# Performance work log

Measured on AMD Instinct MI355X. Metric: run time of the kernel, lower is better.

Reference implementation:

```python
import jax, jax.numpy as jnp
import numpy as np

N_NODES = 100000
N_EDGES = 1600000
NODE_D = 64
EDGE_D = 48
U_D = 32
N_GRAPHS = 64
HIDDEN = 128
OUT_D = 64
IN_D = NODE_D + EDGE_D + U_D  # 144


def setup_inputs() -> dict:
    key = jax.random.key(0)
    ks = jax.random.split(key, 10)
    x = jax.random.normal(ks[0], (N_NODES, NODE_D), dtype=jnp.float32)
    edge_index = jax.random.randint(ks[1], (2, N_EDGES), 0, N_NODES, dtype=jnp.int64)
    edge_attr = jax.random.normal(ks[2], (N_EDGES, EDGE_D), dtype=jnp.float32)
    u = jax.random.normal(ks[3], (N_GRAPHS, U_D), dtype=jnp.float32)
    batch = jnp.sort(jax.random.randint(ks[4], (N_NODES,), 0, N_GRAPHS, dtype=jnp.int64))
    # FCNN params: Linear(144,128) -> relu -> Linear(128,128) -> relu -> Linear(128,64)
    W1 = jax.random.normal(ks[5], (IN_D, HIDDEN), dtype=jnp.float32) / np.sqrt(IN_D)
    b1 = jnp.zeros((HIDDEN,), dtype=jnp.float32)
    W2 = jax.random.normal(ks[6], (HIDDEN, HIDDEN), dtype=jnp.float32) / np.sqrt(HIDDEN)
    b2 = jnp.zeros((HIDDEN,), dtype=jnp.float32)
    W3 = jax.random.normal(ks[7], (HIDDEN, OUT_D), dtype=jnp.float32) / np.sqrt(HIDDEN)
    b3 = jnp.zeros((OUT_D,), dtype=jnp.float32)
    return {"x": x, "edge_index": edge_index, "edge_attr": edge_attr, "u": u,
            "batch": batch, "W1": W1, "b1": b1, "W2": W2, "b2": b2, "W3": W3, "b3": b3}


def reference(x, edge_index, edge_attr, u, batch, W1, b1, W2, b2, W3, b3):
    n = x.shape[0]
    seg = edge_index[0]  # source node per edge
    # scatter_mean(edge_attr, edge_index[0], dim=0) -> [N, edge_d]
    sums = jax.ops.segment_sum(edge_attr, seg, num_segments=n)
    cnt = jax.ops.segment_sum(jnp.ones((edge_attr.shape[0],), edge_attr.dtype), seg, num_segments=n)
    v_e = sums / jnp.maximum(cnt, 1.0)[:, None]  # mean, 0 for empty segments
    comb = jnp.concatenate([x, v_e, u[batch]], axis=1)  # [N, 144]
    h = jax.nn.relu(comb @ W1 + b1)
    h = jax.nn.relu(h @ W2 + b2)
    return h @ W3 + b3
```

## Files before the change

### kernel.cpp

```cpp
#include <hip/hip_runtime.h>
#include <hip/hip_bf16.h>

#define NN 100000
#define NE 1600000
#define NODE_D 64
#define EDGE_D 48
#define U_D 32
#define IN_D 144
#define HID 128
#define OUT_D 64
#define BM 64
#define S0 152
#define SCAN_BS 1024
#define SCAN_NB ((NN + SCAN_BS - 1) / SCAN_BS)
#define W1K 160
#define NW1 (HID * W1K)
#define NW2 (HID * HID)
#define NW3 (OUT_D * HID)
#define NWTOT (NW1 + NW2 + NW3)
#define IDS 1536

typedef __attribute__((ext_vector_type(8))) short bf16x8;
typedef __attribute__((ext_vector_type(4))) float f32x4;

__device__ __forceinline__ short f2bs(float f) {
  union { __hip_bfloat16 h; short s; } v;
  v.h = __float2bfloat16(f);
  return v.s;
}

__device__ __forceinline__ void st4(unsigned short* p, float4 v) {
  unsigned a = (unsigned)(unsigned short)f2bs(v.x) | ((unsigned)(unsigned short)f2bs(v.y) << 16);
  unsigned b = (unsigned)(unsigned short)f2bs(v.z) | ((unsigned)(unsigned short)f2bs(v.w) << 16);
  *reinterpret_cast<uint2*>(p) = make_uint2(a, b);
}

__global__ __launch_bounds__(256) void setup_kernel(
    int* __restrict__ hist,
    const float* __restrict__ W1, const float* __restrict__ W2,
    const float* __restrict__ W3, unsigned short* __restrict__ Wp) {
  const int b = blockIdx.x, tid = threadIdx.x;
  if (b < SCAN_NB) {
    int base = b * SCAN_BS + tid * 4;
    if (base + 3 < NN) {
      *reinterpret_cast<int4*>(&hist[base]) = make_int4(0, 0, 0, 0);
    } else {
      for (int k = 0; k < 4; ++k)
        if (base + k < NN) hist[base + k] = 0;
    }
    return;
  }
  int gid = (b - SCAN_NB) * 256 + tid;
  if (gid >= NWTOT) return;
  float v;
  if (gid < NW1) {
    int n = gid / W1K, k = gid - n * W1K;
    v = (k < IN_D) ? W1[(size_t)k * HID + n] : 0.f;
  } else if (gid < NW1 + NW2) {
    int i2 = gid - NW1;
    int n = i2 >> 7, k = i2 & 127;
    v = W2[(size_t)k * HID + n];
  } else {
    int i3 = gid - NW1 - NW2;
    int n = i3 >> 7, k = i3 & 127;
    v = W3[(size_t)k * OUT_D + n];
  }
  Wp[gid] = (unsigned short)f2bs(v);
}

__global__ __launch_bounds__(256) void hist_kernel(const int* __restrict__ src,
                                                   int* __restrict__ hist) {
  int i = blockIdx.x * 256 + threadIdx.x;
  if (i * 4 >= NE) return;
  int4 s = reinterpret_cast<const int4*>(src)[i];
  atomicAdd(&hist[s.x], 1);
  atomicAdd(&hist[s.y], 1);
  atomicAdd(&hist[s.z], 1);
  atomicAdd(&hist[s.w], 1);
}

__global__ __launch_bounds__(256) void bsum_kernel(const int* __restrict__ hist,
                                                   int* __restrict__ bsum) {
  const int b = blockIdx.x, tid = threadIdx.x;
  const int base = b * SCAN_BS + tid * 4;
  int4 v = make_int4(0, 0, 0, 0);
  if (base + 3 < NN) v = *reinterpret_cast<const int4*>(&hist[base]);
  else {
    int t[4] = {0, 0, 0, 0};
    for (int k = 0; k < 4; ++k) if (base + k < NN) t[k] = hist[base + k];
    v = make_int4(t[0], t[1], t[2], t[3]);
  }
  int s = v.x + v.y + v.z + v.w;
  for (int d = 32; d; d >>= 1) s += __shfl_down(s, d, 64);
  __shared__ int ws[4];
  if ((tid & 63) == 0) ws[tid >> 6] = s;
  __syncthreads();
  if (tid == 0) bsum[b] = ws[0] + ws[1] + ws[2] + ws[3];
}

__global__ __launch_bounds__(128) void bscan_kernel(const int* __restrict__ bsum,
                                                    int* __restrict__ bpre) {
  const int t = threadIdx.x;
  const int lane = t & 63, wave = t >> 6;
  int v = (t < SCAN_NB) ? bsum[t] : 0;
  int incl = v;
  for (int d = 1; d < 64; d <<= 1) {
    int q = __shfl_up(incl, d, 64);
    if (lane >= d) incl += q;
  }
  __shared__ int wtot[2];
  if (lane == 63) wtot[wave] = incl;
  __syncthreads();
  int add = (wave == 1) ? wtot[0] : 0;
  if (t < SCAN_NB) bpre[t] = incl - v + add;
}

__global__ __launch_bounds__(256) void offsets_kernel(const int* __restrict__ hist,
                                                      const int* __restrict__ bpre,
                                                      int* __restrict__ offsets,
                                                      int* __restrict__ cursor) {
  const int b = blockIdx.x, tid = threadIdx.x;
  const int base = b * SCAN_BS + tid * 4;
  const int lane = tid & 63, wave = tid >> 6;
  int4 v = make_int4(0, 0, 0, 0);
  if (base + 3 < NN) v = *reinterpret_cast<const int4*>(&hist[base]);
  else {
    int t[4] = {0, 0, 0, 0};
    for (int k = 0; k < 4; ++k) if (base + k < NN) t[k] = hist[base + k];
    v = make_int4(t[0], t[1], t[2], t[3]);
  }
  const int tsum = v.x + v.y + v.z + v.w;
  int incl = tsum;
  for (int d = 1; d < 64; d <<= 1) {
    int q = __shfl_up(incl, d, 64);
    if (lane >= d) incl += q;
  }
  __shared__ int ws[4];
  __shared__ int wpre[4];
  if (lane == 63) ws[wave] = incl;
  __syncthreads();
  if (tid == 0) {
    int r = 0;
    for (int w = 0; w < 4; ++w) { wpre[w] = r; r += ws[w]; }
  }
  __syncthreads();
  int run = bpre[b] + wpre[wave] + incl - tsum;
  int vals[4] = {v.x, v.y, v.z, v.w};
  for (int k = 0; k < 4; ++k) {
    int i = base + k;
    if (i < NN) { offsets[i] = run; cursor[i] = run; run += vals[k]; }
  }
}

__global__ __launch_bounds__(256) void permute_kernel(const int* __restrict__ src,
                                                      int* __restrict__ cursor,
                                                      int* __restrict__ perm) {
  int i = blockIdx.x * 256 + threadIdx.x;
  if (i * 4 >= NE) return;
  int4 s = reinterpret_cast<const int4*>(src)[i];
  const int e = i * 4;
  int p0 = atomicAdd(&cursor[s.x], 1);
  int p1 = atomicAdd(&cursor[s.y], 1);
  int p2 = atomicAdd(&cursor[s.z], 1);
  int p3 = atomicAdd(&cursor[s.w], 1);
  __builtin_nontemporal_store(e + 0, &perm[p0]);
  __builtin_nontemporal_store(e + 1, &perm[p1]);
  __builtin_nontemporal_store(e + 2, &perm[p2]);
  __builtin_nontemporal_store(e + 3, &perm[p3]);
}

__global__ __launch_bounds__(256) void fused_kernel(
    const float* __restrict__ x, const float* __restrict__ ea,
    const float* __restrict__ u, const int* __restrict__ batch,
    const int* __restrict__ perm, const int* __restrict__ hist,
    const int* __restrict__ offsets, const unsigned short* __restrict__ Wp,
    const float* __restrict__ b1, const float* __restrict__ b2,
    const float* __restrict__ b3, float* __restrict__ out) {
  __shared__ __align__(16) unsigned short act[BM][S0];
  __shared__ int ids[IDS];

  const int tid = threadIdx.x;
  const int lane = tid & 63;
  const int wid = tid >> 6;
  const int lr = lane & 15;
  const int lg = lane >> 4;
  const int node0 = blockIdx.x * BM;

  const unsigned short* Wp1 = Wp;
  const unsigned short* Wp2 = Wp + NW1;
  const unsigned short* Wp3 = Wp + NW1 + NW2;

  const bf16x8 az = {0, 0, 0, 0, 0, 0, 0, 0};

  const int start = offsets[node0];
  const int end = (node0 + BM < NN) ? offsets[node0 + BM] : NE;
  const int L = end - start;
  for (int i = tid; i < L && i < IDS; i += 256)
    ids[i] = perm[start + i];

  for (int i = tid; i < BM * (NODE_D / 4); i += 256) {
    int r = i >> 4, q = i & 15;
    int node = node0 + r;
    float4 v = make_float4(0.f, 0.f, 0.f, 0.f);
    if (node < NN) v = reinterpret_cast<const float4*>(x)[(size_t)node * 16 + q];
    st4(&act[r][q * 4], v);
  }
  for (int i = tid; i < BM * (U_D / 4); i += 256) {
    int r = i >> 3, q = i & 7;
    int node = node0 + r;
    float4 v = make_float4(0.f, 0.f, 0.f, 0.f);
    if (node < NN) {
      int b = batch[node];
      v = reinterpret_cast<const float4*>(u)[(size_t)b * 8 + q];
    }
    st4(&act[r][NODE_D + EDGE_D + q * 4], v);
  }
  __syncthreads();

  {
    const int g = tid >> 4;
    const int c = tid & 15;
    const bool on = (c < 12);
    const float* bc = ea + (size_t)c * 4;
    for (int i = 0; i < 4; ++i) {
      const int nl = g * 4 + i;
      const int node = node0 + nl;
      int deg = 0, sl = 0;
      if (node < NN) { deg = hist[node]; sl = offsets[node] - start; }
      float4 a0 = make_float4(0.f, 0.f, 0.f, 0.f);
      float4 a1 = make_float4(0.f, 0.f, 0.f, 0.f);
      int j = 0;
      for (; j + 7 < deg; j += 8) {
        int p = sl + j;
        int e0 = (p + 0 < IDS) ? ids[p + 0] : perm[start + p + 0];
        int e1 = (p + 1 < IDS) ? ids[p + 1] : perm[start + p + 1];
        int e2 = (p + 2 < IDS) ? ids[p + 2] : perm[start + p + 2];
        int e3 = (p + 3 < IDS) ? ids[p + 3] : perm[start + p + 3];
        int e4 = (p + 4 < IDS) ? ids[p + 4] : perm[start + p + 4];
        int e5 = (p + 5 < IDS) ? ids[p + 5] : perm[start + p + 5];
        int e6 = (p + 6 < IDS) ? ids[p + 6] : perm[start + p + 6];
        int e7 = (p + 7 < IDS) ? ids[p + 7] : perm[start + p + 7];
        if (on) {
          float4 v0 = *reinterpret_cast<const float4*>(bc + (size_t)e0 * EDGE_D);
          float4 v1 = *reinterpret_cast<const float4*>(bc + (size_t)e1 * EDGE_D);
          float4 v2 = *reinterpret_cast<const float4*>(bc + (size_t)e2 * EDGE_D);
          float4 v3 = *reinterpret_cast<const float4*>(bc + (size_t)e3 * EDGE_D);
          float4 v4 = *reinterpret_cast<const float4*>(bc + (size_t)e4 * EDGE_D);
          float4 v5 = *reinterpret_cast<const float4*>(bc + (size_t)e5 * EDGE_D);
          float4 v6 = *reinterpret_cast<const float4*>(bc + (size_t)e6 * EDGE_D);
          float4 v7 = *reinterpret_cast<const float4*>(bc + (size_t)e7 * EDGE_D);
          a0.x += (v0.x + v1.x) + (v2.x + v3.x);
          a0.y += (v0.y + v1.y) + (v2.y + v3.y);
          a0.z += (v0.z + v1.z) + (v2.z + v3.z);
          a0.w += (v0.w + v1.w) + (v2.w + v3.w);
          a1.x += (v4.x + v5.x) + (v6.x + v7.x);
          a1.y += (v4.y + v5.y) + (v6.y + v7.y);
          a1.z += (v4.z + v5.z) + (v6.z + v7.z);
          a1.w += (v4.w + v5.w) + (v6.w + v7.w);
        }
      }
      for (; j + 3 < deg; j += 4) {
        int p = sl + j;
        int e0 = (p + 0 < IDS) ? ids[p + 0] : perm[start + p + 0];
        int e1 = (p + 1 < IDS) ? ids[p + 1] : perm[start + p + 1];
        int e2 = (p + 2 < IDS) ? ids[p + 2] : perm[start + p + 2];
        int e3 = (p + 3 < IDS) ? ids[p + 3] : perm[start + p + 3];
        if (on) {
          float4 v0 = *reinterpret_cast<const float4*>(bc + (size_t)e0 * EDGE_D);
          float4 v1 = *reinterpret_cast<const float4*>(bc + (size_t)e1 * EDGE_D);
          float4 v2 = *reinterpret_cast<const float4*>(bc + (size_t)e2 * EDGE_D);
          float4 v3 = *reinterpret_cast<const float4*>(bc + (size_t)e3 * EDGE_D);
          a0.x += (v0.x + v1.x) + (v2.x + v3.x);
          a0.y += (v0.y + v1.y) + (v2.y + v3.y);
          a0.z += (v0.z + v1.z) + (v2.z + v3.z);
          a0.w += (v0.w + v1.w) + (v2.w + v3.w);
        }
      }
      for (; j < deg; ++j) {
        int p = sl + j;
        int e0 = (p < IDS) ? ids[p] : perm[start + p];
        if (on) {
          float4 v0 = *reinterpret_cast<const float4*>(bc + (size_t)e0 * EDGE_D);
          a0.x += v0.x; a0.y += v0.y; a0.z += v0.z; a0.w += v0.w;
        }
      }
      float inv = (deg > 0) ? 1.0f / (float)deg : 0.0f;
      if (on && node < NN)
        st4(&act[nl][NODE_D + c * 4],
            make_float4((a0.x + a1.x) * inv, (a0.y + a1.y) * inv,
                        (a0.z + a1.z) * inv, (a0.w + a1.w) * inv));
    }
  }
  __syncthreads();

  {
    const int n0 = wid * 32;
    bf16x8 wf[5][2];
#pragma unroll
    for (int t = 0; t < 5; ++t)
#pragma unroll
      for (int nf = 0; nf < 2; ++nf)
        wf[t][nf] = *reinterpret_cast<const bf16x8*>(
            &Wp1[(size_t)(n0 + nf * 16 + lr) * W1K + t * 32 + lg * 8]);
    float bias0 = b1[n0 + lr], bias1 = b1[n0 + 16 + lr];
    f32x4 acc[4][2];
#pragma unroll
    for (int mf = 0; mf < 4; ++mf) {
      acc[mf][0] = (f32x4){bias0, bias0, bias0, bias0};
      acc[mf][1] = (f32x4){bias1, bias1, bias1, bias1};
    }
#pragma unroll
    for (int t = 0; t < 5; ++t) {
#pragma unroll
      for (int mf = 0; mf < 4; ++mf) {
        bf16x8 a;
        if (t < 4) {
          a = *reinterpret_cast<const bf16x8*>(&act[mf * 16 + lr][t * 32 + lg * 8]);
        } else {
          a = az;
          if (lg < 2)
            a = *reinterpret_cast<const bf16x8*>(&act[mf * 16 + lr][128 + lg * 8]);
        }
        acc[mf][0] = __builtin_amdgcn_mfma_f32_16x16x32_bf16(a, wf[t][0], acc[mf][0], 0, 0, 0);
        acc[mf][1] = __builtin_amdgcn_mfma_f32_16x16x32_bf16(a, wf[t][1], acc[mf][1], 0, 0, 0);
      }
    }
    __syncthreads();
#pragma unroll
    for (int mf = 0; mf < 4; ++mf)
#pragma unroll
      for (int nf = 0; nf < 2; ++nf)
#pragma unroll
        for (int r = 0; r < 4; ++r)
          act[mf * 16 + lg * 4 + r][n0 + nf * 16 + lr] =
              (unsigned short)f2bs(fmaxf(acc[mf][nf][r], 0.f));
  }
  __syncthreads();

  {
    const int n0 = wid * 32;
    bf16x8 wf[4][2];
#pragma unroll
    for (int t = 0; t < 4; ++t)
#pragma unroll
      for (int nf = 0; nf < 2; ++nf)
        wf[t][nf] = *reinterpret_cast<const bf16x8*>(
            &Wp2[(size_t)(n0 + nf * 16 + lr) * HID + t * 32 + lg * 8]);
    float bias0 = b2[n0 + lr], bias1 = b2[n0 + 16 + lr];
    f32x4 acc[4][2];
#pragma unroll
    for (int mf = 0; mf < 4; ++mf) {
      acc[mf][0] = (f32x4){bias0, bias0, bias0, bias0};
      acc[mf][1] = (f32x4){bias1, bias1, bias1, bias1};
    }
#pragma unroll
    for (int t = 0; t < 4; ++t) {
#pragma unroll
      for (int mf = 0; mf < 4; ++mf) {
        bf16x8 a = *reinterpret_cast<const bf16x8*>(&act[mf * 16 + lr][t * 32 + lg * 8]);
        acc[mf][0] = __builtin_amdgcn_mfma_f32_16x16x32_bf16(a, wf[t][0], acc[mf][0], 0, 0, 0);
        acc[mf][1] = __builtin_amdgcn_mfma_f32_16x16x32_bf16(a, wf[t][1], acc[mf][1], 0, 0, 0);
      }
    }
    __syncthreads();
#pragma unroll
    for (int mf = 0; mf < 4; ++mf)
#pragma unroll
      for (int nf = 0; nf < 2; ++nf)
#pragma unroll
        for (int r = 0; r < 4; ++r)
          act[mf * 16 + lg * 4 + r][n0 + nf * 16 + lr] =
              (unsigned short)f2bs(fmaxf(acc[mf][nf][r], 0.f));
  }
  __syncthreads();

  {
    const int n0 = wid * 16;
    bf16x8 wf[4];
#pragma unroll
    for (int t = 0; t < 4; ++t)
      wf[t] = *reinterpret_cast<const bf16x8*>(
          &Wp3[(size_t)(n0 + lr) * HID + t * 32 + lg * 8]);
    float bias = b3[n0 + lr];
    f32x4 acc[4];
#pragma unroll
    for (int mf = 0; mf < 4; ++mf) acc[mf] = (f32x4){bias, bias, bias, bias};
#pragma unroll
    for (int t = 0; t < 4; ++t) {
#pragma unroll
      for (int mf = 0; mf < 4; ++mf) {
        bf16x8 a = *reinterpret_cast<const bf16x8*>(&act[mf * 16 + lr][t * 32 + lg * 8]);
        acc[mf] = __builtin_amdgcn_mfma_f32_16x16x32_bf16(a, wf[t], acc[mf], 0, 0, 0);
      }
    }
#pragma unroll
    for (int mf = 0; mf < 4; ++mf)
#pragma unroll
      for (int r = 0; r < 4; ++r) {
        int node = node0 + mf * 16 + lg * 4 + r;
        if (node < NN) out[(size_t)node * OUT_D + n0 + lr] = acc[mf][r];
      }
  }
}

extern "C" void kernel_launch(void* const* d_in, const int* in_sizes, int n_in,
                              void* d_out, int out_size, void* d_ws, size_t ws_size,
                              hipStream_t stream) {
  const float* x   = (const float*)d_in[0];
  const int* ei    = (const int*)d_in[1];
  const float* ea  = (const float*)d_in[2];
  const float* u   = (const float*)d_in[3];
  const int* batch = (const int*)d_in[4];
  const float* W1  = (const float*)d_in[5];
  const float* b1  = (const float*)d_in[6];
  const float* W2  = (const float*)d_in[7];
  const float* b2  = (const float*)d_in[8];
  const float* W3  = (const float*)d_in[9];
  const float* b3  = (const float*)d_in[10];
  float* out = (float*)d_out;

  int* hist    = (int*)d_ws;
  int* offsets = hist + NN;
  int* cursor  = offsets + NN;
  int* perm    = cursor + NN;
  int* bsum    = perm + NE;
  int* bpre    = bsum + SCAN_NB;
  unsigned short* Wp = (unsigned short*)(bpre + SCAN_NB + 60);

  const int wblocks = (NWTOT + 255) / 256;
  const int e4blocks = (NE / 4 + 255) / 256;
  setup_kernel<<<SCAN_NB + wblocks, 256, 0, stream>>>(hist, W1, W2, W3, Wp);
  hist_kernel<<<e4blocks, 256, 0, stream>>>(ei, hist);
  bsum_kernel<<<SCAN_NB, 256, 0, stream>>>(hist, bsum);
  bscan_kernel<<<1, 128, 0, stream>>>(bsum, bpre);
  offsets_kernel<<<SCAN_NB, 256, 0, stream>>>(hist, bpre, offsets, cursor);
  permute_kernel<<<e4blocks, 256, 0, stream>>>(ei, cursor, perm);
  fused_kernel<<<(NN + BM - 1) / BM, 256, 0, stream>>>(
      x, ea, u, batch, perm, hist, offsets, Wp, b1, b2, b3, out);
}
```

Measured before the change: 318.1 us.

## Scatter edge features into CSR-sorted bf16 buffer instead of index permutation

Instead of building a permutation of edge ids and gathering fp32 edge rows by index in the fused kernel, the permute stage now reads each edge's fp32 feature row and writes it as bf16 into its sorted CSR slot. The fused kernel then reads each node's edges contiguously in bf16, dropping the shared-memory id staging, the perm lookups and one barrier. The edge array is read once in its original order, then written and re-read at half width. The cost is an extra 154MB-class scatter write pass plus a larger workspace, and edge features are rounded to bf16 before averaging, which adds rounding error.

```diff
diff --git a/kernel.cpp b/kernel.cpp
--- a/kernel.cpp
+++ b/kernel.cpp
@@ -18,15 +18,21 @@
 #define NW2 (HID * HID)
 #define NW3 (OUT_D * HID)
 #define NWTOT (NW1 + NW2 + NW3)
-#define IDS 1536
 
 typedef __attribute__((ext_vector_type(8))) short bf16x8;
 typedef __attribute__((ext_vector_type(4))) float f32x4;
+typedef __attribute__((ext_vector_type(4))) unsigned int u32x4;
 
 __device__ __forceinline__ short f2bs(float f) {
   union { __hip_bfloat16 h; short s; } v;
   v.h = __float2bfloat16(f);
   return v.s;
+}
+__device__ __forceinline__ float blo(unsigned int pk) {
+  union { unsigned int u; float f; } v; v.u = pk << 16; return v.f;
+}
+__device__ __forceinline__ float bhi(unsigned int pk) {
+  union { unsigned int u; float f; } v; v.u = pk & 0xffff0000u; return v.f;
 }
 
 __device__ __forceinline__ void st4(unsigned short* p, float4 v) {
@@ -152,32 +158,41 @@
   }
 }
 
-__global__ __launch_bounds__(256) void permute_kernel(const int* __restrict__ src,
-                                                      int* __restrict__ cursor,
-                                                      int* __restrict__ perm) {
-  int i = blockIdx.x * 256 + threadIdx.x;
-  if (i * 4 >= NE) return;
-  int4 s = reinterpret_cast<const int4*>(src)[i];
-  const int e = i * 4;
-  int p0 = atomicAdd(&cursor[s.x], 1);
-  int p1 = atomicAdd(&cursor[s.y], 1);
-  int p2 = atomicAdd(&cursor[s.z], 1);
-  int p3 = atomicAdd(&cursor[s.w], 1);
-  __builtin_nontemporal_store(e + 0, &perm[p0]);
-  __builtin_nontemporal_store(e + 1, &perm[p1]);
-  __builtin_nontemporal_store(e + 2, &perm[p2]);
-  __builtin_nontemporal_store(e + 3, &perm[p3]);
+__global__ __launch_bounds__(256) void permute_data_kernel(
+    const int* __restrict__ src, const float* __restrict__ ea,
+    int* __restrict__ cursor, unsigned short* __restrict__ ea16) {
+  int e = blockIdx.x * 256 + threadIdx.x;
+  if (e >= NE) return;
+  int s = src[e];
+  int pos = atomicAdd(&cursor[s], 1);
+  const float4* rp = reinterpret_cast<const float4*>(ea + (size_t)e * EDGE_D);
+  float4 v[12];
+#pragma unroll
+  for (int k = 0; k < 12; ++k) v[k] = rp[k];
+  unsigned short* dst = ea16 + (size_t)pos * EDGE_D;
+#pragma unroll
+  for (int k = 0; k < 6; ++k) {
+    u32x4 w;
+    w.x = (unsigned)(unsigned short)f2bs(v[2 * k].x) |
+          ((unsigned)(unsigned short)f2bs(v[2 * k].y) << 16);
+    w.y = (unsigned)(unsigned short)f2bs(v[2 * k].z) |
+          ((unsigned)(unsigned short)f2bs(v[2 * k].w) << 16);
+    w.z = (unsigned)(unsigned short)f2bs(v[2 * k + 1].x) |
+          ((unsigned)(unsigned short)f2bs(v[2 * k + 1].y) << 16);
+    w.w = (unsigned)(unsigned short)f2bs(v[2 * k + 1].z) |
+          ((unsigned)(unsigned short)f2bs(v[2 * k + 1].w) << 16);
+    __builtin_nontemporal_store(w, reinterpret_cast<u32x4*>(dst) + k);
+  }
 }
 
 __global__ __launch_bounds__(256) void fused_kernel(
-    const float* __restrict__ x, const float* __restrict__ ea,
+    const float* __restrict__ x, const unsigned short* __restrict__ ea16,
     const float* __restrict__ u, const int* __restrict__ batch,
-    const int* __restrict__ perm, const int* __restrict__ hist,
-    const int* __restrict__ offsets, const unsigned short* __restrict__ Wp,
+    const int* __restrict__ hist, const int* __restrict__ offsets,
+    const unsigned short* __restrict__ Wp,
     const float* __restrict__ b1, const float* __restrict__ b2,
     const float* __restrict__ b3, float* __restrict__ out) {
   __shared__ __align__(16) unsigned short act[BM][S0];
-  __shared__ int ids[IDS];
 
   const int tid = threadIdx.x;
   const int lane = tid & 63;
@@ -191,12 +206,6 @@
   const unsigned short* Wp3 = Wp + NW1 + NW2;
 
   const bf16x8 az = {0, 0, 0, 0, 0, 0, 0, 0};
-
-  const int start = offsets[node0];
-  const int end = (node0 + BM < NN) ? offsets[node0 + BM] : NE;
-  const int L = end - start;
-  for (int i = tid; i < L && i < IDS; i += 256)
-    ids[i] = perm[start + i];
 
   for (int i = tid; i < BM * (NODE_D / 4); i += 256) {
     int r = i >> 4, q = i & 15;
@@ -215,73 +224,57 @@
     }
     st4(&act[r][NODE_D + EDGE_D + q * 4], v);
   }
-  __syncthreads();
 
   {
     const int g = tid >> 4;
     const int c = tid & 15;
     const bool on = (c < 12);
-    const float* bc = ea + (size_t)c * 4;
     for (int i = 0; i < 4; ++i) {
       const int nl = g * 4 + i;
       const int node = node0 + nl;
-      int deg = 0, sl = 0;
-      if (node < NN) { deg = hist[node]; sl = offsets[node] - start; }
+      int deg = 0, off = 0;
+      if (node < NN) { deg = hist[node]; off = offsets[node]; }
+      const unsigned short* rp = ea16 + (size_t)off * EDGE_D + c * 4;
       float4 a0 = make_float4(0.f, 0.f, 0.f, 0.f);
       float4 a1 = make_float4(0.f, 0.f, 0.f, 0.f);
       int j = 0;
       for (; j + 7 < deg; j += 8) {
-        int p = sl + j;
-        int e0 = (p + 0 < IDS) ? ids[p + 0] : perm[start + p + 0];
-        int e1 = (p + 1 < IDS) ? ids[p + 1] : perm[start + p + 1];
-        int e2 = (p + 2 < IDS) ? ids[p + 2] : perm[start + p + 2];
-        int e3 = (p + 3 < IDS) ? ids[p + 3] : perm[start + p + 3];
-        int e4 = (p + 4 < IDS) ? ids[p + 4] : perm[start + p + 4];
-        int e5 = (p + 5 < IDS) ? ids[p + 5] : perm[start + p + 5];
-        int e6 = (p + 6 < IDS) ? ids[p + 6] : perm[start + p + 6];
-        int e7 = (p + 7 < IDS) ? ids[p + 7] : perm[start + p + 7];
         if (on) {
-          float4 v0 = *reinterpret_cast<const float4*>(bc + (size_t)e0 * EDGE_D);
-          float4 v1 = *reinterpret_cast<const float4*>(bc + (size_t)e1 * EDGE_D);
-          float4 v2 = *reinterpret_cast<const float4*>(bc + (size_t)e2 * EDGE_D);
-          float4 v3 = *reinterpret_cast<const float4*>(bc + (size_t)e3 * EDGE_D);
-          float4 v4 = *reinterpret_cast<const float4*>(bc + (size_t)e4 * EDGE_D);
-          float4 v5 = *reinterpret_cast<const float4*>(bc + (size_t)e5 * EDGE_D);
-          float4 v6 = *reinterpret_cast<const float4*>(bc + (size_t)e6 * EDGE_D);
-          float4 v7 = *reinterpret_cast<const float4*>(bc + (size_t)e7 * EDGE_D);
-          a0.x += (v0.x + v1.x) + (v2.x + v3.x);
-          a0.y += (v0.y + v1.y) + (v2.y + v3.y);
-          a0.z += (v0.z + v1.z) + (v2.z + v3.z);
-          a0.w += (v0.w + v1.w) + (v2.w + v3.w);
-          a1.x += (v4.x + v5.x) + (v6.x + v7.x);
-          a1.y += (v4.y + v5.y) + (v6.y + v7.y);
-          a1.z += (v4.z + v5.z) + (v6.z + v7.z);
-          a1.w += (v4.w + v5.w) + (v6.w + v7.w);
+          uint2 w0 = *reinterpret_cast<const uint2*>(rp + (size_t)(j + 0) * EDGE_D);
+          uint2 w1 = *reinterpret_cast<const uint2*>(rp + (size_t)(j + 1) * EDGE_D);
+          uint2 w2 = *reinterpret_cast<const uint2*>(rp + (size_t)(j + 2) * EDGE_D);
+          uint2 w3 = *reinterpret_cast<const uint2*>(rp + (size_t)(j + 3) * EDGE_D);
+          uint2 w4 = *reinterpret_cast<const uint2*>(rp + (size_t)(j + 4) * EDGE_D);
+          uint2 w5 = *reinterpret_cast<const uint2*>(rp + (size_t)(j + 5) * EDGE_D);
+          uint2 w6 = *reinterpret_cast<const uint2*>(rp + (size_t)(j + 6) * EDGE_D);
+          uint2 w7 = *reinterpret_cast<const uint2*>(rp + (size_t)(j + 7) * EDGE_D);
+          a0.x += blo(w0.x) + blo(w1.x) + blo(w2.x) + blo(w3.x);
+          a0.y += bhi(w0.x) + bhi(w1.x) + bhi(w2.x) + bhi(w3.x);
+          a0.z += blo(w0.y) + blo(w1.y) + blo(w2.y) + blo(w3.y);
+          a0.w += bhi(w0.y) + bhi(w1.y) + bhi(w2.y) + bhi(w3.y);
+          a1.x += blo(w4.x) + blo(w5.x) + blo(w6.x) + blo(w7.x);
+          a1.y += bhi(w4.x) + bhi(w5.x) + bhi(w6.x) + bhi(w7.x);
+          a1.z += blo(w4.y) + blo(w5.y) + blo(w6.y) + blo(w7.y);
+          a1.w += bhi(w4.y) + bhi(w5.y) + bhi(w6.y) + bhi(w7.y);
         }
       }
       for (; j + 3 < deg; j += 4) {
-        int p = sl + j;
-        int e0 = (p + 0 < IDS) ? ids[p + 0] : perm[start + p + 0];
-        int e1 = (p + 1 < IDS) ? ids[p + 1] : perm[start + p + 1];
-        int e2 = (p + 2 < IDS) ? ids[p + 2] : perm[start + p + 2];
-        int e3 = (p + 3 < IDS) ? ids[p + 3] : perm[start + p + 3];
         if (on) {
-          float4 v0 = *reinterpret_cast<const float4*>(bc + (size_t)e0 * EDGE_D);
-          float4 v1 = *reinterpret_cast<const float4*>(bc + (size_t)e1 * EDGE_D);
-          float4 v2 = *reinterpret_cast<const float4*>(bc + (size_t)e2 * EDGE_D);
-          float4 v3 = *reinterpret_cast<const float4*>(bc + (size_t)e3 * EDGE_D);
-          a0.x += (v0.x + v1.x) + (v2.x + v3.x);
-          a0.y += (v0.y + v1.y) + (v2.y + v3.y);
-          a0.z += (v0.z + v1.z) + (v2.z + v3.z);
-          a0.w += (v0.w + v1.w) + (v2.w + v3.w);
+          uint2 w0 = *reinterpret_cast<const uint2*>(rp + (size_t)(j + 0) * EDGE_D);
+          uint2 w1 = *reinterpret_cast<const uint2*>(rp + (size_t)(j + 1) * EDGE_D);
+          uint2 w2 = *reinterpret_cast<const uint2*>(rp + (size_t)(j + 2) * EDGE_D);
+          uint2 w3 = *reinterpret_cast<const uint2*>(rp + (size_t)(j + 3) * EDGE_D);
+          a0.x += blo(w0.x) + blo(w1.x) + blo(w2.x) + blo(w3.x);
+          a0.y += bhi(w0.x) + bhi(w1.x) + bhi(w2.x) + bhi(w3.x);
+          a0.z += blo(w0.y) + blo(w1.y) + blo(w2.y) + blo(w3.y);
+          a0.w += bhi(w0.y) + bhi(w1.y) + bhi(w2.y) + bhi(w3.y);
         }
       }
       for (; j < deg; ++j) {
-        int p = sl + j;
-        int e0 = (p < IDS) ? ids[p] : perm[start + p];
         if (on) {
-          float4 v0 = *reinterpret_cast<const float4*>(bc + (size_t)e0 * EDGE_D);
-          a0.x += v0.x; a0.y += v0.y; a0.z += v0.z; a0.w += v0.w;
+          uint2 w0 = *reinterpret_cast<const uint2*>(rp + (size_t)j * EDGE_D);
+          a0.x += blo(w0.x); a0.y += bhi(w0.x);
+          a0.z += blo(w0.y); a0.w += bhi(w0.y);
         }
       }
       float inv = (deg > 0) ? 1.0f / (float)deg : 0.0f;
@@ -419,11 +412,11 @@
   const float* b3  = (const float*)d_in[10];
   float* out = (float*)d_out;
 
-  int* hist    = (int*)d_ws;
+  unsigned short* ea16 = (unsigned short*)d_ws;
+  int* hist    = (int*)(ea16 + (size_t)NE * EDGE_D);
   int* offsets = hist + NN;
   int* cursor  = offsets + NN;
-  int* perm    = cursor + NN;
-  int* bsum    = perm + NE;
+  int* bsum    = cursor + NN;
   int* bpre    = bsum + SCAN_NB;
   unsigned short* Wp = (unsigned short*)(bpre + SCAN_NB + 60);
 
@@ -434,7 +427,7 @@
   bsum_kernel<<<SCAN_NB, 256, 0, stream>>>(hist, bsum);
   bscan_kernel<<<1, 128, 0, stream>>>(bsum, bpre);
   offsets_kernel<<<SCAN_NB, 256, 0, stream>>>(hist, bpre, offsets, cursor);
-  permute_kernel<<<e4blocks, 256, 0, stream>>>(ei, cursor, perm);
+  permute_data_kernel<<<(NE + 255) / 256, 256, 0, stream>>>(ei, ea, cursor, ea16);
   fused_kernel<<<(NN + BM - 1) / BM, 256, 0, stream>>>(
-      x, ea, u, batch, perm, hist, offsets, Wp, b1, b2, b3, out);
-}
+      x, ea16, u, batch, hist, offsets, Wp, b1, b2, b3, out);
+}
```

New measurement: 461.6 us. +45.1%, slower.
